# Optimization experiments

Hardware: AMD Instinct MI355X
Metric: run time of the kernel (lower is better)

Reference implementation:

```python
import jax, jax.numpy as jnp
import numpy as np

NUM_HEADS = 8

def conv1x1(x, w, b):
    # x: [B,C,H,W], w: [O,C], b: [O]
    return jnp.einsum('bchw,oc->bohw', x, w) + b[None, :, None, None]

def setup_inputs() -> dict:
    key = jax.random.key(0)
    ks = jax.random.split(key, 8)
    B, C, H, W = 8, 256, 32, 32
    HF, WF = 128, 128
    s = 1.0 / np.sqrt(C)  # xavier-ish scale for 1x1 convs
    return {
        'x': jax.random.normal(ks[0], (B, C, H, W), jnp.float32),
        'featmap': jax.random.normal(ks[1], (B, C, HF, WF), jnp.float32),
        'wq': jax.random.normal(ks[2], (C, C), jnp.float32) * s,
        'bq': jnp.zeros((C,), jnp.float32),
        'wk': jax.random.normal(ks[3], (C, C), jnp.float32) * s,
        'bk': jnp.zeros((C,), jnp.float32),
        'wv': jax.random.normal(ks[4], (C, C), jnp.float32) * s,
        'bv': jnp.zeros((C,), jnp.float32),
        'wg': jax.random.normal(ks[5], (1, C), jnp.float32) * s,
        'bg': jnp.zeros((1,), jnp.float32),
    }

def _to_grid(t, h, w, rh, rw):
    # t: [B8, d, h*rh, w*rw] -> [B8, d, h, w, rh*rw] (aligned local grid per query pixel)
    b8, d = t.shape[:2]
    t = t.reshape(b8, d, h, rh, w, rw)
    return t.transpose(0, 1, 2, 4, 3, 5).reshape(b8, d, h, w, rh * rw)

def reference(x, featmap, wq, bq, wk, bk, wv, bv, wg, bg):
    B, C, H, W = x.shape
    HF, WF = featmap.shape[2:]
    head_dim = C // NUM_HEADS
    scaling = float(head_dim) ** -0.5
    rh, rw = HF // H, WF // W

    grid_weight = jax.nn.sigmoid(conv1x1(x, wg, bg))          # [B,1,H,W]
    q = conv1x1(x, wq, bq) * scaling                           # [B,C,H,W]
    k = conv1x1(featmap, wk, bk)                               # [B,C,HF,WF]
    v = conv1x1(featmap, wv, bv)

    q = q.reshape(B * NUM_HEADS, head_dim, H, W)
    k = k.reshape(B * NUM_HEADS, head_dim, HF, WF)
    v = v.reshape(B * NUM_HEADS, head_dim, HF, WF)

    k_grid = _to_grid(k, H, W, rh, rw)                         # [B8,d,H,W,P]
    v_grid = _to_grid(v, H, W, rh, rw)

    # ga_align_weight: correlate each query pixel with its aligned key grid
    attn = jnp.einsum('bchw,bchwp->bphw', q, k_grid)           # [B8,P,H,W]
    attn = jax.nn.softmax(attn, axis=1)
    # ga_align_map: weighted sum of aligned value grid
    out = jnp.einsum('bphw,bchwp->bchw', attn, v_grid)         # [B8,d,H,W]

    out = out.reshape(B, C, H, W) * grid_weight
    return out
```

## Files before the change

kernel.cpp:

```cpp
#include <hip/hip_runtime.h>

#define CDIM 256
#define SCALING 0.17677669529663687f

typedef _Float16 f16;
typedef f16 f16x4 __attribute__((ext_vector_type(4)));
typedef f16 f16x8 __attribute__((ext_vector_type(8)));
typedef float f32x4 __attribute__((ext_vector_type(4)));

#define MFMA(a, b, c) __builtin_amdgcn_mfma_f32_16x16x32_f16(a, b, c, 0, 0, 0)

__device__ __forceinline__ unsigned pack2(float a, float b) {
  union { f16 h[2]; unsigned u; } r;
  r.h[0] = (f16)a;
  r.h[1] = (f16)b;
  return r.u;
}

__global__ __launch_bounds__(256) void k_prep_w2(const float* __restrict__ wq,
                                                 const float* __restrict__ bq,
                                                 const float* __restrict__ wk,
                                                 const float* __restrict__ wv,
                                                 f16* __restrict__ W2h,
                                                 float* __restrict__ b2,
                                                 f16* __restrict__ wvh) {
  __shared__ float wk_s[32][8];
  const int t = threadIdx.x, ciO = blockIdx.x, hd = blockIdx.y;
  {
    int j = t >> 3, c8 = t & 7;
    wk_s[j][c8] = wk[(hd * 32 + j) * CDIM + ciO * 8 + c8];
    int idx = (hd * 32 + j) * CDIM + ciO * 8 + c8;
    wvh[idx] = (f16)wv[idx];
  }
  float wq_r[32];
#pragma unroll
  for (int j = 0; j < 32; ++j) wq_r[j] = wq[(hd * 32 + j) * CDIM + t];
  __syncthreads();
  for (int c8 = 0; c8 < 8; ++c8) {
    float acc = 0.f;
#pragma unroll
    for (int j = 0; j < 32; ++j) acc = fmaf(wq_r[j], wk_s[j][c8], acc);
    W2h[(size_t)(hd * CDIM + ciO * 8 + c8) * CDIM + t] = (f16)(acc * SCALING);
  }
  if (t < 8) {
    float a = 0.f;
    for (int j = 0; j < 32; ++j) a = fmaf(wk_s[j][t], bq[hd * 32 + j], a);
    b2[hd * CDIM + ciO * 8 + t] = a * SCALING;
  }
}

__global__ __launch_bounds__(256, 2) void k_qkw2(const float* __restrict__ x,
                                                 const f16* __restrict__ W2h,
                                                 const float* __restrict__ b2,
                                                 const float* __restrict__ wg,
                                                 const float* __restrict__ bg,
                                                 f16* __restrict__ qk,
                                                 float* __restrict__ gw, int b0) {
  __shared__ __align__(16) f16 A_l[256 * 40];
  __shared__ __align__(16) f16 B_l[64 * 40];
  const int t = threadIdx.x;
  const int p16 = blockIdx.x, hd = blockIdx.y, bz = blockIdx.z;
  const int bb = b0 + bz;
  const int lane = t & 63, wid = t >> 6, l15 = lane & 15, h4 = lane >> 4;
  f32x4 acc[4][4] = {};
  float gacc = 0.f;

  for (int kb = 0; kb < 8; ++kb) {
    __syncthreads();
#pragma unroll
    for (int it = 0; it < 4; ++it) {
      int e = it * 256 + t, ci = e >> 2, q = e & 3;
      *(f16x8*)(A_l + ci * 40 + q * 8) =
          *(const f16x8*)(W2h + (size_t)(hd * CDIM + ci) * CDIM + kb * 32 + q * 8);
    }
#pragma unroll
    for (int it = 0; it < 2; ++it) {
      int e = it * 256 + t, cx = e >> 4, p4 = e & 15;
      float4 v = *(const float4*)(x + (size_t)(bb * CDIM + kb * 32 + cx) * 1024 +
                                  p16 * 64 + p4 * 4);
      B_l[(p4 * 4 + 0) * 40 + cx] = (f16)v.x;
      B_l[(p4 * 4 + 1) * 40 + cx] = (f16)v.y;
      B_l[(p4 * 4 + 2) * 40 + cx] = (f16)v.z;
      B_l[(p4 * 4 + 3) * 40 + cx] = (f16)v.w;
    }
    __syncthreads();
    if (hd == 0 && wid == 3) {
#pragma unroll
      for (int cx = 0; cx < 32; ++cx)
        gacc = fmaf(wg[kb * 32 + cx], (float)B_l[lane * 40 + cx], gacc);
    }
    f16x8 a[4], bf[4];
#pragma unroll
    for (int mt = 0; mt < 4; ++mt)
      a[mt] = *(const f16x8*)(A_l + (wid * 64 + mt * 16 + l15) * 40 + h4 * 8);
#pragma unroll
    for (int nt = 0; nt < 4; ++nt)
      bf[nt] = *(const f16x8*)(B_l + (nt * 16 + l15) * 40 + h4 * 8);
#pragma unroll
    for (int mt = 0; mt < 4; ++mt)
#pragma unroll
      for (int nt = 0; nt < 4; ++nt) acc[mt][nt] = MFMA(a[mt], bf[nt], acc[mt][nt]);
  }
#pragma unroll
  for (int mt = 0; mt < 4; ++mt) {
    int ci0 = wid * 64 + mt * 16 + h4 * 4;
    float4 bvv = *(const float4*)(b2 + hd * CDIM + ci0);
#pragma unroll
    for (int nt = 0; nt < 4; ++nt) {
      int pix = p16 * 64 + nt * 16 + l15;
      union { f16 h[4]; unsigned long long u; } P;
      P.h[0] = (f16)(acc[mt][nt][0] + bvv.x);
      P.h[1] = (f16)(acc[mt][nt][1] + bvv.y);
      P.h[2] = (f16)(acc[mt][nt][2] + bvv.z);
      P.h[3] = (f16)(acc[mt][nt][3] + bvv.w);
      *(unsigned long long*)(qk + ((size_t)(bz * 1024 + pix) * 8 + hd) * CDIM + ci0) = P.u;
    }
  }
  if (hd == 0 && wid == 3)
    gw[bz * 1024 + p16 * 64 + lane] = 1.f / (1.f + __expf(-(gacc + bg[0])));
}

__global__ __launch_bounds__(256, 4) void k_attn(const float* __restrict__ feat,
                                                 const f16* __restrict__ qk,
                                                 f16* __restrict__ fa, int b0) {
  __shared__ __align__(16) f16 cip[4 * 4608];
  __shared__ __align__(16) f16 attn_l[4 * 512];
  const int t = threadIdx.x;
  const int h = blockIdx.x, w4 = blockIdx.y, bz = blockIdx.z;
  const int bb = b0 + bz;
  const int lane = t & 63, w = t >> 6, l15 = lane & 15, h4 = lane >> 4;
  const int pixb = h * 32 + w4 * 4;

  const float* fb = feat + (size_t)bb * (CDIM * 16384) + (h * 4) * 128 + w4 * 16;
  float4 fv[8];
#pragma unroll
  for (int it = 0; it < 8; ++it) {
    int e = it * 256 + t, px = e & 3, r = (e >> 2) & 3, ci = e >> 4;
    fv[it] = *(const float4*)(fb + (size_t)ci * 16384 + r * 128 + px * 4);
  }
  const f16* qkg = qk + ((size_t)(bz * 1024 + pixb + w) * 8 + (l15 & 7)) * CDIM;
  f16x8 apre[8];
#pragma unroll
  for (int kb = 0; kb < 8; ++kb) apre[kb] = *(const f16x8*)(qkg + kb * 32 + h4 * 8);
  {
    f16x8 z = {};
    *(f16x8*)(attn_l + t * 8) = z;
  }
#pragma unroll
  for (int it = 0; it < 4; ++it) {
    int e = it * 256 + t, px = e >> 8, ci = e & 255;
    *(unsigned*)(cip + px * 4608 + ci * 18 + 16) = 0;
  }
#pragma unroll
  for (int it = 0; it < 8; ++it) {
    int e = it * 256 + t, px = e & 3, r = (e >> 2) & 3, ci = e >> 4;
    uint2 pk;
    pk.x = pack2(fv[it].x, fv[it].y);
    pk.y = pack2(fv[it].z, fv[it].w);
    *(uint2*)(cip + px * 4608 + ci * 18 + r * 4) = pk;
  }
#pragma unroll
  for (int it = 8; it < 16; ++it) {
    int e = it * 256 + t, px = e & 3, r = (e >> 2) & 3, ci = e >> 4;
    float4 v = *(const float4*)(fb + (size_t)ci * 16384 + r * 128 + px * 4);
    uint2 pk;
    pk.x = pack2(v.x, v.y);
    pk.y = pack2(v.z, v.w);
    *(uint2*)(cip + px * 4608 + ci * 18 + r * 4) = pk;
  }
  __syncthreads();

  const f16* cw = cip + w * 4608;
  f32x4 acc = {};
#pragma unroll
  for (int kb = 0; kb < 8; ++kb) {
    f16x8 bf;
#pragma unroll
    for (int j = 0; j < 8; ++j) bf[j] = cw[(kb * 32 + h4 * 8 + j) * 18 + l15];
    acc = MFMA(apre[kb], bf, acc);
  }
  float at[4];
#pragma unroll
  for (int r = 0; r < 4; ++r) {
    float m = acc[r];
    m = fmaxf(m, __shfl_xor(m, 1, 64));
    m = fmaxf(m, __shfl_xor(m, 2, 64));
    m = fmaxf(m, __shfl_xor(m, 4, 64));
    m = fmaxf(m, __shfl_xor(m, 8, 64));
    float e = __expf(acc[r] - m);
    float s = e;
    s += __shfl_xor(s, 1, 64);
    s += __shfl_xor(s, 2, 64);
    s += __shfl_xor(s, 4, 64);
    s += __shfl_xor(s, 8, 64);
    at[r] = e / s;
  }
  if (h4 < 2) {
#pragma unroll
    for (int r = 0; r < 4; ++r) attn_l[w * 512 + l15 * 16 + h4 * 4 + r] = (f16)at[r];
  }
  f16x8 b5;
#pragma unroll
  for (int j = 0; j < 8; ++j) b5[j] = attn_l[w * 512 + (h4 * 8 + j) * 16 + l15];
  const f32x4 zero = {};
#pragma unroll
  for (int nt = 0; nt < 16; ++nt) {
    const unsigned* ap = (const unsigned*)(cw + (nt * 16 + l15) * 18 + h4 * 8);
    union { unsigned u[4]; f16x8 h; } A;
    A.u[0] = ap[0]; A.u[1] = ap[1]; A.u[2] = ap[2]; A.u[3] = ap[3];
    f32x4 d = MFMA(A.h, b5, zero);
    if (l15 < 8) {
      union { f16 h[4]; unsigned long long u; } P;
      P.h[0] = (f16)d[0]; P.h[1] = (f16)d[1]; P.h[2] = (f16)d[2]; P.h[3] = (f16)d[3];
      *(unsigned long long*)(fa + ((size_t)(bz * 8 + l15) * 1024 + pixb + w) * CDIM +
                             nt * 16 + h4 * 4) = P.u;
    }
  }
}

__global__ __launch_bounds__(256) void k_out(const f16* __restrict__ fa,
                                             const f16* __restrict__ wvh,
                                             const float* __restrict__ bv,
                                             const float* __restrict__ gw,
                                             float* __restrict__ out, int b0) {
  __shared__ __align__(16) f16 wv_l[32 * 264];
  const int t = threadIdx.x;
  const int p16 = blockIdx.x, hd = blockIdx.y, bz = blockIdx.z;
  const int bb = b0 + bz;
  const int lane = t & 63, wid = t >> 6, l15 = lane & 15, h4 = lane >> 4;

  const f16* fap = fa + ((size_t)(bz * 8 + hd) * 1024 + p16 * 64 + wid * 16 + l15) * CDIM +
                   h4 * 8;
  f16x8 apre[8];
#pragma unroll
  for (int kb = 0; kb < 8; ++kb) apre[kb] = *(const f16x8*)(fap + kb * 32);
  int pix0 = p16 * 64 + wid * 16 + h4 * 4;
  float4 g = *(const float4*)(gw + bz * 1024 + pix0);

#pragma unroll
  for (int it = 0; it < 4; ++it) {
    int e = it * 256 + t, c = e >> 5, ch = e & 31;
    *(f16x8*)(wv_l + c * 264 + ch * 8) =
        *(const f16x8*)(wvh + (size_t)(hd * 32 + c) * CDIM + ch * 8);
  }
  __syncthreads();
  f32x4 acc[2] = {};
#pragma unroll
  for (int kb = 0; kb < 8; ++kb) {
#pragma unroll
    for (int nt = 0; nt < 2; ++nt) {
      f16x8 b = *(const f16x8*)(wv_l + (nt * 16 + l15) * 264 + kb * 32 + h4 * 8);
      acc[nt] = MFMA(apre[kb], b, acc[nt]);
    }
  }
#pragma unroll
  for (int nt = 0; nt < 2; ++nt) {
    int c = hd * 32 + nt * 16 + l15;
    float bvc = bv[c];
    float4 o;
    o.x = (acc[nt][0] + bvc) * g.x;
    o.y = (acc[nt][1] + bvc) * g.y;
    o.z = (acc[nt][2] + bvc) * g.z;
    o.w = (acc[nt][3] + bvc) * g.w;
    *(float4*)(out + (size_t)(bb * CDIM + c) * 1024 + pix0) = o;
  }
}

extern "C" void kernel_launch(void* const* d_in, const int* in_sizes, int n_in,
                              void* d_out, int out_size, void* d_ws, size_t ws_size,
                              hipStream_t stream) {
  const float* x = (const float*)d_in[0];
  const float* feat = (const float*)d_in[1];
  const float* wq = (const float*)d_in[2];
  const float* bq = (const float*)d_in[3];
  const float* wk = (const float*)d_in[4];
  const float* wv = (const float*)d_in[6];
  const float* bv = (const float*)d_in[7];
  const float* wg = (const float*)d_in[8];
  const float* bg = (const float*)d_in[9];
  float* out = (float*)d_out;

  char* ws = (char*)d_ws;
  f16* W2h = (f16*)ws;
  float* b2 = (float*)(ws + 1048576);
  f16* wvh = (f16*)(ws + 1056768);
  char* dyn = ws + 1187840;

  k_prep_w2<<<dim3(32, 8), 256, 0, stream>>>(wq, bq, wk, wv, W2h, b2, wvh);

  const size_t QK = 4194304, FA = 4194304, GW = 4096;
  if (ws_size >= 1187840 + 8 * (QK + FA + GW)) {
    f16* qkp = (f16*)dyn;
    f16* fap = (f16*)(dyn + 8 * QK);
    float* gwp = (float*)(dyn + 8 * (QK + FA));
    k_qkw2<<<dim3(16, 8, 8), 256, 0, stream>>>(x, W2h, b2, wg, bg, qkp, gwp, 0);
    k_attn<<<dim3(32, 8, 8), 256, 0, stream>>>(feat, qkp, fap, 0);
    k_out<<<dim3(16, 8, 8), 256, 0, stream>>>(fap, wvh, bv, gwp, out, 0);
  } else {
    f16* qkp = (f16*)dyn;
    f16* fap = (f16*)(dyn + QK);
    float* gwp = (float*)(dyn + QK + FA);
    for (int b = 0; b < 8; ++b) {
      k_qkw2<<<dim3(16, 8, 1), 256, 0, stream>>>(x, W2h, b2, wg, bg, qkp, gwp, b);
      k_attn<<<dim3(32, 8, 1), 256, 0, stream>>>(feat, qkp, fap, b);
      k_out<<<dim3(16, 8, 1), 256, 0, stream>>>(fap, wvh, bv, gwp, out, b);
    }
  }
}
```

Baseline: 79.13 us.

## Fuse value projection output GEMM into attention kernel, drop intermediate buffer

The k_out kernel is folded into k_attn. Per-head attention results are staged in shared memory (reusing the cip buffer at an offset) instead of written to a global fp16 buffer, then multiplied by the value weights, with bias and the grid gate applied inside the same kernel. This removes a kernel launch and the global write and read of the intermediate. In exchange, occupancy is lowered to 3 waves per SIMD, wvh is read from global/L2 by every block, and the output stores become scalar with only 4 of 16 lanes active, which may hurt coalescing.

Measured after the change: 88.34 us. 11.6% more time.

```diff
diff --git a/kernel.cpp b/kernel.cpp
--- a/kernel.cpp
+++ b/kernel.cpp
@@ -120,9 +120,13 @@
     gw[bz * 1024 + p16 * 64 + lane] = 1.f / (1.f + __expf(-(gacc + bg[0])));
 }
 
-__global__ __launch_bounds__(256, 4) void k_attn(const float* __restrict__ feat,
+#define FAOFF 2496
+__global__ __launch_bounds__(256, 3) void k_attn(const float* __restrict__ feat,
                                                  const f16* __restrict__ qk,
-                                                 f16* __restrict__ fa, int b0) {
+                                                 const f16* __restrict__ wvh,
+                                                 const float* __restrict__ bv,
+                                                 const float* __restrict__ gw,
+                                                 float* __restrict__ out, int b0) {
   __shared__ __align__(16) f16 cip[4 * 4608];
   __shared__ __align__(16) f16 attn_l[4 * 512];
   const int t = threadIdx.x;
@@ -203,66 +207,52 @@
 #pragma unroll
   for (int j = 0; j < 8; ++j) b5[j] = attn_l[w * 512 + (h4 * 8 + j) * 16 + l15];
   const f32x4 zero = {};
+  unsigned long long dpk[16];
 #pragma unroll
   for (int nt = 0; nt < 16; ++nt) {
     const unsigned* ap = (const unsigned*)(cw + (nt * 16 + l15) * 18 + h4 * 8);
     union { unsigned u[4]; f16x8 h; } A;
     A.u[0] = ap[0]; A.u[1] = ap[1]; A.u[2] = ap[2]; A.u[3] = ap[3];
     f32x4 d = MFMA(A.h, b5, zero);
-    if (l15 < 8) {
-      union { f16 h[4]; unsigned long long u; } P;
-      P.h[0] = (f16)d[0]; P.h[1] = (f16)d[1]; P.h[2] = (f16)d[2]; P.h[3] = (f16)d[3];
-      *(unsigned long long*)(fa + ((size_t)(bz * 8 + l15) * 1024 + pixb + w) * CDIM +
-                             nt * 16 + h4 * 4) = P.u;
-    }
-  }
-}
-
-__global__ __launch_bounds__(256) void k_out(const f16* __restrict__ fa,
-                                             const f16* __restrict__ wvh,
-                                             const float* __restrict__ bv,
-                                             const float* __restrict__ gw,
-                                             float* __restrict__ out, int b0) {
-  __shared__ __align__(16) f16 wv_l[32 * 264];
-  const int t = threadIdx.x;
-  const int p16 = blockIdx.x, hd = blockIdx.y, bz = blockIdx.z;
-  const int bb = b0 + bz;
-  const int lane = t & 63, wid = t >> 6, l15 = lane & 15, h4 = lane >> 4;
-
-  const f16* fap = fa + ((size_t)(bz * 8 + hd) * 1024 + p16 * 64 + wid * 16 + l15) * CDIM +
-                   h4 * 8;
-  f16x8 apre[8];
-#pragma unroll
-  for (int kb = 0; kb < 8; ++kb) apre[kb] = *(const f16x8*)(fap + kb * 32);
-  int pix0 = p16 * 64 + wid * 16 + h4 * 4;
-  float4 g = *(const float4*)(gw + bz * 1024 + pix0);
-
-#pragma unroll
-  for (int it = 0; it < 4; ++it) {
-    int e = it * 256 + t, c = e >> 5, ch = e & 31;
-    *(f16x8*)(wv_l + c * 264 + ch * 8) =
-        *(const f16x8*)(wvh + (size_t)(hd * 32 + c) * CDIM + ch * 8);
+    union { f16 h[4]; unsigned long long u; } P;
+    P.h[0] = (f16)d[0]; P.h[1] = (f16)d[1]; P.h[2] = (f16)d[2]; P.h[3] = (f16)d[3];
+    dpk[nt] = P.u;
+  }
+  __builtin_amdgcn_sched_barrier(0);
+  if (l15 < 8) {
+    f16* faw = cip + w * 4608 + FAOFF + l15 * 264;
+#pragma unroll
+    for (int nt = 0; nt < 16; ++nt)
+      *(unsigned long long*)(faw + nt * 16 + h4 * 4) = dpk[nt];
   }
   __syncthreads();
-  f32x4 acc[2] = {};
-#pragma unroll
-  for (int kb = 0; kb < 8; ++kb) {
-#pragma unroll
-    for (int nt = 0; nt < 2; ++nt) {
-      f16x8 b = *(const f16x8*)(wv_l + (nt * 16 + l15) * 264 + kb * 32 + h4 * 8);
-      acc[nt] = MFMA(apre[kb], b, acc[nt]);
-    }
-  }
-#pragma unroll
-  for (int nt = 0; nt < 2; ++nt) {
-    int c = hd * 32 + nt * 16 + l15;
-    float bvc = bv[c];
-    float4 o;
-    o.x = (acc[nt][0] + bvc) * g.x;
-    o.y = (acc[nt][1] + bvc) * g.y;
-    o.z = (acc[nt][2] + bvc) * g.z;
-    o.w = (acc[nt][3] + bvc) * g.w;
-    *(float4*)(out + (size_t)(bb * CDIM + c) * 1024 + pix0) = o;
+
+  {
+    const float gwv = gw[bz * 1024 + pixb + (l15 & 3)];
+#pragma unroll
+    for (int hd2 = 0; hd2 < 2; ++hd2) {
+      const int hd = w * 2 + hd2;
+      const f16* fab = cip + (l15 & 3) * 4608 + FAOFF + hd * 264;
+#pragma unroll
+      for (int mt = 0; mt < 2; ++mt) {
+        f32x4 acc6 = {};
+#pragma unroll
+        for (int kb = 0; kb < 8; ++kb) {
+          f16x8 a6 = *(const f16x8*)(wvh + (size_t)(hd * 32 + mt * 16 + l15) * CDIM +
+                                     kb * 32 + h4 * 8);
+          f16x8 b6 = *(const f16x8*)(fab + kb * 32 + h4 * 8);
+          acc6 = MFMA(a6, b6, acc6);
+        }
+        if (l15 < 4) {
+          const int c0 = hd * 32 + mt * 16 + h4 * 4;
+          float4 bv4 = *(const float4*)(bv + c0);
+          out[(size_t)(bb * CDIM + c0 + 0) * 1024 + pixb + l15] = (acc6[0] + bv4.x) * gwv;
+          out[(size_t)(bb * CDIM + c0 + 1) * 1024 + pixb + l15] = (acc6[1] + bv4.y) * gwv;
+          out[(size_t)(bb * CDIM + c0 + 2) * 1024 + pixb + l15] = (acc6[2] + bv4.z) * gwv;
+          out[(size_t)(bb * CDIM + c0 + 3) * 1024 + pixb + l15] = (acc6[3] + bv4.w) * gwv;
+        }
+      }
+    }
   }
 }
 
@@ -288,22 +278,18 @@
 
   k_prep_w2<<<dim3(32, 8), 256, 0, stream>>>(wq, bq, wk, wv, W2h, b2, wvh);
 
-  const size_t QK = 4194304, FA = 4194304, GW = 4096;
-  if (ws_size >= 1187840 + 8 * (QK + FA + GW)) {
+  const size_t QK = 4194304, GW = 4096;
+  if (ws_size >= 1187840 + 8 * (QK + GW)) {
     f16* qkp = (f16*)dyn;
-    f16* fap = (f16*)(dyn + 8 * QK);
-    float* gwp = (float*)(dyn + 8 * (QK + FA));
+    float* gwp = (float*)(dyn + 8 * QK);
     k_qkw2<<<dim3(16, 8, 8), 256, 0, stream>>>(x, W2h, b2, wg, bg, qkp, gwp, 0);
-    k_attn<<<dim3(32, 8, 8), 256, 0, stream>>>(feat, qkp, fap, 0);
-    k_out<<<dim3(16, 8, 8), 256, 0, stream>>>(fap, wvh, bv, gwp, out, 0);
+    k_attn<<<dim3(32, 8, 8), 256, 0, stream>>>(feat, qkp, wvh, bv, gwp, out, 0);
   } else {
     f16* qkp = (f16*)dyn;
-    f16* fap = (f16*)(dyn + QK);
-    float* gwp = (float*)(dyn + QK + FA);
+    float* gwp = (float*)(dyn + QK);
     for (int b = 0; b < 8; ++b) {
       k_qkw2<<<dim3(16, 8, 1), 256, 0, stream>>>(x, W2h, b2, wg, bg, qkp, gwp, b);
-      k_attn<<<dim3(32, 8, 1), 256, 0, stream>>>(feat, qkp, fap, b);
-      k_out<<<dim3(16, 8, 1), 256, 0, stream>>>(fap, wvh, bv, gwp, out, b);
-    }
-  }
-}
+      k_attn<<<dim3(32, 8, 1), 256, 0, stream>>>(feat, qkp, wvh, bv, gwp, out, b);
+    }
+  }
+}
```

## Pretranspose x to f16 pixel-major buffer and drop LDS staging in qk GEMM

Applied to the files above, without the earlier changes.

Adds a k_xt kernel that converts x to f16 and transposes it to pixel-major layout, and moves the grid-weight sigmoid there. k_qkw2 then loads MFMA operands straight from global memory (W2h and xT) without LDS staging or barriers. The intent is to stop each of the 8 head blocks from re-converting and re-transposing the same x tile, and to remove the sync overhead. The cost is an extra launch, an extra 4 MB of intermediate traffic, and operand loads from global memory that rely on caching.

Result: slower. 98.13 us (+24.0%).

```diff
diff --git a/kernel.cpp b/kernel.cpp
--- a/kernel.cpp
+++ b/kernel.cpp
@@ -49,53 +49,59 @@
   }
 }
 
-__global__ __launch_bounds__(256, 2) void k_qkw2(const float* __restrict__ x,
+__global__ __launch_bounds__(256) void k_xt(const float* __restrict__ x,
+                                            const float* __restrict__ wg,
+                                            const float* __restrict__ bg,
+                                            f16* __restrict__ xT,
+                                            float* __restrict__ gw, int b0) {
+  __shared__ f16 tile[32][260];
+  const int t = threadIdx.x;
+  const int pT = blockIdx.x, bz = blockIdx.y;
+  const int bb = b0 + bz;
+  const float* xb = x + (size_t)bb * (CDIM * 1024) + pT * 32;
+#pragma unroll
+  for (int it = 0; it < 8; ++it) {
+    int e = it * 256 + t, p4 = e & 7, cx = e >> 3;
+    float4 v = *(const float4*)(xb + (size_t)cx * 1024 + p4 * 4);
+    tile[p4 * 4 + 0][cx] = (f16)v.x;
+    tile[p4 * 4 + 1][cx] = (f16)v.y;
+    tile[p4 * 4 + 2][cx] = (f16)v.z;
+    tile[p4 * 4 + 3][cx] = (f16)v.w;
+  }
+  __syncthreads();
+  f16* xTb = xT + (size_t)bz * (1024 * CDIM) + pT * 32 * CDIM;
+#pragma unroll
+  for (int it = 0; it < 4; ++it) {
+    int e = it * 256 + t, cxo = e & 31, pix = e >> 5;
+    *(f16x8*)(xTb + pix * CDIM + cxo * 8) = *(const f16x8*)(&tile[pix][cxo * 8]);
+  }
+  if (t < 32) {
+    float a = 0.f;
+    for (int cx = 0; cx < CDIM; ++cx) a = fmaf((float)tile[t][cx], wg[cx], a);
+    gw[bz * 1024 + pT * 32 + t] = 1.f / (1.f + __expf(-(a + bg[0])));
+  }
+}
+
+__global__ __launch_bounds__(256, 2) void k_qkw2(const f16* __restrict__ xT,
                                                  const f16* __restrict__ W2h,
                                                  const float* __restrict__ b2,
-                                                 const float* __restrict__ wg,
-                                                 const float* __restrict__ bg,
-                                                 f16* __restrict__ qk,
-                                                 float* __restrict__ gw, int b0) {
-  __shared__ __align__(16) f16 A_l[256 * 40];
-  __shared__ __align__(16) f16 B_l[64 * 40];
+                                                 f16* __restrict__ qk, int b0) {
   const int t = threadIdx.x;
   const int p16 = blockIdx.x, hd = blockIdx.y, bz = blockIdx.z;
-  const int bb = b0 + bz;
   const int lane = t & 63, wid = t >> 6, l15 = lane & 15, h4 = lane >> 4;
+  const f16* Whd = W2h + (size_t)hd * CDIM * CDIM;
+  const f16* xTb = xT + (size_t)bz * (1024 * CDIM) + (size_t)(p16 * 64) * CDIM;
   f32x4 acc[4][4] = {};
-  float gacc = 0.f;
 
   for (int kb = 0; kb < 8; ++kb) {
-    __syncthreads();
-#pragma unroll
-    for (int it = 0; it < 4; ++it) {
-      int e = it * 256 + t, ci = e >> 2, q = e & 3;
-      *(f16x8*)(A_l + ci * 40 + q * 8) =
-          *(const f16x8*)(W2h + (size_t)(hd * CDIM + ci) * CDIM + kb * 32 + q * 8);
-    }
-#pragma unroll
-    for (int it = 0; it < 2; ++it) {
-      int e = it * 256 + t, cx = e >> 4, p4 = e & 15;
-      float4 v = *(const float4*)(x + (size_t)(bb * CDIM + kb * 32 + cx) * 1024 +
-                                  p16 * 64 + p4 * 4);
-      B_l[(p4 * 4 + 0) * 40 + cx] = (f16)v.x;
-      B_l[(p4 * 4 + 1) * 40 + cx] = (f16)v.y;
-      B_l[(p4 * 4 + 2) * 40 + cx] = (f16)v.z;
-      B_l[(p4 * 4 + 3) * 40 + cx] = (f16)v.w;
-    }
-    __syncthreads();
-    if (hd == 0 && wid == 3) {
-#pragma unroll
-      for (int cx = 0; cx < 32; ++cx)
-        gacc = fmaf(wg[kb * 32 + cx], (float)B_l[lane * 40 + cx], gacc);
-    }
     f16x8 a[4], bf[4];
 #pragma unroll
     for (int mt = 0; mt < 4; ++mt)
-      a[mt] = *(const f16x8*)(A_l + (wid * 64 + mt * 16 + l15) * 40 + h4 * 8);
+      a[mt] = *(const f16x8*)(Whd + (size_t)(wid * 64 + mt * 16 + l15) * CDIM + kb * 32 +
+                              h4 * 8);
 #pragma unroll
     for (int nt = 0; nt < 4; ++nt)
-      bf[nt] = *(const f16x8*)(B_l + (nt * 16 + l15) * 40 + h4 * 8);
+      bf[nt] = *(const f16x8*)(xTb + (size_t)(nt * 16 + l15) * CDIM + kb * 32 + h4 * 8);
 #pragma unroll
     for (int mt = 0; mt < 4; ++mt)
 #pragma unroll
@@ -116,8 +122,6 @@
       *(unsigned long long*)(qk + ((size_t)(bz * 1024 + pix) * 8 + hd) * CDIM + ci0) = P.u;
     }
   }
-  if (hd == 0 && wid == 3)
-    gw[bz * 1024 + p16 * 64 + lane] = 1.f / (1.f + __expf(-(gacc + bg[0])));
 }
 
 __global__ __launch_bounds__(256, 4) void k_attn(const float* __restrict__ feat,
@@ -288,20 +292,24 @@
 
   k_prep_w2<<<dim3(32, 8), 256, 0, stream>>>(wq, bq, wk, wv, W2h, b2, wvh);
 
-  const size_t QK = 4194304, FA = 4194304, GW = 4096;
-  if (ws_size >= 1187840 + 8 * (QK + FA + GW)) {
-    f16* qkp = (f16*)dyn;
-    f16* fap = (f16*)(dyn + 8 * QK);
-    float* gwp = (float*)(dyn + 8 * (QK + FA));
-    k_qkw2<<<dim3(16, 8, 8), 256, 0, stream>>>(x, W2h, b2, wg, bg, qkp, gwp, 0);
+  const size_t XT = 4194304, QK = 4194304, FA = 4194304, GW = 4096;
+  if (ws_size >= 1187840 + 8 * (XT / 8 * 0 + QK + FA + GW) + 8 * 524288 + 4194304) {
+    f16* xT = (f16*)dyn;
+    f16* qkp = (f16*)(dyn + 4194304);
+    f16* fap = (f16*)(dyn + 4194304 + 8 * QK);
+    float* gwp = (float*)(dyn + 4194304 + 8 * QK + 8 * FA);
+    k_xt<<<dim3(32, 8), 256, 0, stream>>>(x, wg, bg, xT, gwp, 0);
+    k_qkw2<<<dim3(16, 8, 8), 256, 0, stream>>>(xT, W2h, b2, qkp, 0);
     k_attn<<<dim3(32, 8, 8), 256, 0, stream>>>(feat, qkp, fap, 0);
     k_out<<<dim3(16, 8, 8), 256, 0, stream>>>(fap, wvh, bv, gwp, out, 0);
   } else {
-    f16* qkp = (f16*)dyn;
-    f16* fap = (f16*)(dyn + QK);
-    float* gwp = (float*)(dyn + QK + FA);
+    f16* xT = (f16*)dyn;
+    f16* qkp = (f16*)(dyn + 524288);
+    f16* fap = (f16*)(dyn + 524288 + QK);
+    float* gwp = (float*)(dyn + 524288 + QK + FA);
     for (int b = 0; b < 8; ++b) {
-      k_qkw2<<<dim3(16, 8, 1), 256, 0, stream>>>(x, W2h, b2, wg, bg, qkp, gwp, b);
+      k_xt<<<dim3(32, 1), 256, 0, stream>>>(x, wg, bg, xT, gwp, b);
+      k_qkw2<<<dim3(16, 8, 1), 256, 0, stream>>>(xT, W2h, b2, qkp, b);
       k_attn<<<dim3(32, 8, 1), 256, 0, stream>>>(feat, qkp, fap, b);
       k_out<<<dim3(16, 8, 1), 256, 0, stream>>>(fap, wvh, bv, gwp, out, b);
     }
```
